# Kernel optimization log

Hardware: AMD Instinct MI355X
Metric: run time of the kernel (lower is better)

The kernel has to match this reference:

```python
import math
import jax, jax.numpy as jnp
import numpy as np

WS = 4            # window size
LS = 2 * WS       # local context size
NH = 8            # num heads
DIM = 128
EPS = 1e-5


def setup_inputs() -> dict:
    key = jax.random.key(0)
    ks = jax.random.split(key, 8)
    B, C, H, W = 4, DIM, 48, 48
    features = jax.random.normal(ks[0], (B, C, H, W), dtype=jnp.float32)
    s = 0.02
    return {
        'features': features,
        'ln_w': jnp.ones((C,), jnp.float32),
        'ln_b': jnp.zeros((C,), jnp.float32),
        'q_w': jax.random.normal(ks[1], (C, C), jnp.float32) * s,
        'q_b': jnp.zeros((C,), jnp.float32),
        'kv_w': jax.random.normal(ks[2], (2 * C, C), jnp.float32) * s,
        'kv_b': jnp.zeros((2 * C,), jnp.float32),
        'out_w': jax.random.normal(ks[3], (C, C), jnp.float32) * s,
        'out_b': jnp.zeros((C,), jnp.float32),
    }


def _avgpool_tokens(x, k):
    # x: [B,C,H,W] -> [B, (H//k)*(W//k), C]
    B, C, H, W = x.shape
    t = x.reshape(B, C, H // k, k, W // k, k).mean(axis=(3, 5))
    return t.reshape(B, C, -1).transpose(0, 2, 1)


def reference(features, ln_w, ln_b, q_w, q_b, kv_w, kv_b, out_w, out_b):
    B, C, H, W = features.shape
    Hw, Ww = H // WS, W // WS
    nw = Hw * Ww
    hd = C // NH

    # ---- window partition: [B,C,H,W] -> [B*nw, WS*WS, C]
    qt = features.reshape(B, C, Hw, WS, Ww, WS).transpose(0, 2, 4, 3, 5, 1)
    qt = qt.reshape(B * nw, WS * WS, C)

    # ---- LayerNorm(dim)
    mu = qt.mean(-1, keepdims=True)
    var = qt.var(-1, keepdims=True)
    qt = (qt - mu) / jnp.sqrt(var + EPS) * ln_w + ln_b

    # ---- local context: pad to target, unfold kernel=LS stride=WS
    target = (int(math.sqrt(nw)) - 1) * WS + LS
    ph, pw = max(0, target - H), max(0, target - W)
    pad = ((0, 0), (0, 0), (ph // 2, ph - ph // 2), (pw // 2, pw - pw // 2))
    padded = jnp.pad(features, pad)
    # channel order of patches is (C, kh, kw), same as torch unfold
    patches = jax.lax.conv_general_dilated_patches(
        padded, filter_shape=(LS, LS), window_strides=(WS, WS), padding='VALID')
    local = patches.reshape(B, C, LS * LS, nw).transpose(0, 3, 2, 1)
    local = local.reshape(B * nw, LS * LS, C)

    # ---- multi-scale pooled tokens, broadcast to each window
    mid = _avgpool_tokens(features, 2)      # [B, M, C]
    glo = _avgpool_tokens(features, 4)      # [B, G, C]
    mid = jnp.broadcast_to(mid[:, None], (B, nw) + mid.shape[1:]).reshape(B * nw, -1, C)
    glo = jnp.broadcast_to(glo[:, None], (B, nw) + glo.shape[1:]).reshape(B * nw, -1, C)

    kv_tokens = jnp.concatenate([local, mid, glo], axis=1)  # [B*nw, Nkv, C]

    # ---- projections (torch Linear: x @ W.T + b)
    queries = qt @ q_w.T + q_b
    kv = kv_tokens @ kv_w.T + kv_b
    keys, values = kv[..., :C], kv[..., C:]

    # ---- multi-head attention
    Nq, Nkv = queries.shape[1], keys.shape[1]
    q = queries.reshape(-1, Nq, NH, hd)
    k = keys.reshape(-1, Nkv, NH, hd)
    v = values.reshape(-1, Nkv, NH, hd)
    scores = jnp.einsum('bqhd,bkhd->bhqk', q, k) / math.sqrt(hd)
    weights = jax.nn.softmax(scores, axis=-1)
    attended = jnp.einsum('bhqk,bkhd->bqhd', weights, v).reshape(-1, Nq, C)

    out = attended @ out_w.T + out_b

    # ---- window reconstruction -> [B,C,H,W]
    out = out.reshape(B, Hw, Ww, WS, WS, C).transpose(0, 5, 1, 3, 2, 4)
    out = out.reshape(B, C, H, W)
    return out + features
```

## Files before the change

kernel.cpp:

```cpp
#include <hip/hip_runtime.h>


typedef unsigned short u16;
typedef short v8s __attribute__((ext_vector_type(8)));
typedef v8s __attribute__((may_alias)) v8s_am;
typedef short v4s __attribute__((ext_vector_type(4)));
typedef v4s __attribute__((may_alias)) v4s_am;
typedef float v4f __attribute__((ext_vector_type(4)));

#define MFMA_BF16(a, b, c) __builtin_amdgcn_mfma_f32_16x16x32_bf16(a, b, c, 0, 0, 0)

#if __has_builtin(__builtin_amdgcn_mfma_f32_16x16x16bf16_1k)
#define MFMA16(a, b, c) __builtin_amdgcn_mfma_f32_16x16x16bf16_1k(a, b, c, 0, 0, 0)
#else
static __device__ __forceinline__ v4f mfma16_fb(v4s a, v4s b, v4f c) {
    v8s a8 = {a[0], a[1], a[2], a[3], 0, 0, 0, 0};
    v8s b8 = {b[0], b[1], b[2], b[3], 0, 0, 0, 0};
    return MFMA_BF16(a8, b8, c);
}
#define MFMA16(a, b, c) mfma16_fb(a, b, c)
#endif

#if __has_builtin(__builtin_amdgcn_exp2f)
#define EXP2(x) __builtin_amdgcn_exp2f(x)
#else
#define EXP2(x) exp2f(x)
#endif

__device__ __forceinline__ float b2f(u16 u) {
    union { unsigned int i; float f; } x;
    x.i = ((unsigned int)u) << 16;
    return x.f;
}
__device__ __forceinline__ u16 f2b(float f) {
    union { float f; unsigned int i; } x;
    x.f = f;
    unsigned int u = x.i;
    return (u16)((u + 0x7fffu + ((u >> 16) & 1u)) >> 16);
}

__global__ __launch_bounds__(256) void k_prep(
    const float* __restrict__ F,
    const float* __restrict__ qw, const float* __restrict__ kvw,
    const float* __restrict__ ow,
    const float* __restrict__ lnw, const float* __restrict__ lnb,
    const float* __restrict__ kvb,
    u16* __restrict__ Xt, u16* __restrict__ Xln, u16* __restrict__ Wb,
    u16* __restrict__ Pml, u16* __restrict__ Vlh)
{
    int blk = blockIdx.x;
    int t = threadIdx.x;
    if (blk >= 484) {
        int base = (blk - 484) * 8192 + t * 32;
#pragma unroll
        for (int k = 0; k < 4; ++k) {
            int off = base + k * 8;
            int ch = off / 10816;
            u16 bv = f2b(kvb[128 + ch]);
            v8s o = {(short)bv, (short)bv, (short)bv, (short)bv,
                     (short)bv, (short)bv, (short)bv, (short)bv};
            *(v8s_am*)&Vlh[off] = o;
        }
        return;
    }
    if (blk >= 304) {
        int gid = (blk - 304) * 256 + t;
        int row = gid >> 4;
        int seg = gid & 15;
        v8s outv;
        if (row < 2304) {
            int b = row / 576, r = row % 576;
            int i = r / 24, j = r % 24;
#pragma unroll
            for (int jc = 0; jc < 8; ++jc) {
                int c = seg * 8 + jc;
                const float* src = F + ((size_t)(b * 128 + c)) * 2304 + (2 * i) * 48 + 2 * j;
                float2 a = *(const float2*)src;
                float2 d = *(const float2*)(src + 48);
                outv[jc] = (short)f2b((a.x + a.y + d.x + d.y) * 0.25f);
            }
        } else {
            int r2 = row - 2304;
            int b = r2 / 144, r = r2 % 144;
            int i = r / 12, j = r % 12;
#pragma unroll
            for (int jc = 0; jc < 8; ++jc) {
                int c = seg * 8 + jc;
                const float* src = F + ((size_t)(b * 128 + c)) * 2304 + (4 * i) * 48 + 4 * j;
                float s = 0.f;
#pragma unroll
                for (int di = 0; di < 4; ++di) {
                    float4 v = *(const float4*)(src + di * 48);
                    s += (v.x + v.y) + (v.z + v.w);
                }
                outv[jc] = (short)f2b(s * 0.0625f);
            }
        }
        *(v8s_am*)&Pml[((size_t)row) * 128 + seg * 8] = outv;
        return;
    }
    if (blk >= 288) {
        int base = (blk - 288) * 4096 + t * 16;
#pragma unroll
        for (int i = 0; i < 4; ++i) {
            int idx = base + i * 4;
            const float* src; int off;
            if (idx < 16384)      { src = qw;  off = idx; }
            else if (idx < 49152) { src = kvw; off = idx - 16384; }
            else                  { src = ow;  off = idx - 49152; }
            float4 v = *(const float4*)(src + off);
            unsigned long long packed =
                (unsigned long long)f2b(v.x) |
                ((unsigned long long)f2b(v.y) << 16) |
                ((unsigned long long)f2b(v.z) << 32) |
                ((unsigned long long)f2b(v.w) << 48);
            *(unsigned long long*)(Wb + idx) = packed;
        }
        if (blk == 288) {
            Wb[65536 + t] = f2b(t < 128 ? lnw[t] : lnb[t - 128]);
            Wb[65792 + t] = f2b(kvb[t]);
        }
        return;
    }
    __shared__ u16 X[128][34];
    __shared__ float Lw[128], Lb[128];
    if (t < 128) Lw[t] = lnw[t];
    else         Lb[t - 128] = lnb[t - 128];
    int b = blk / 72;
    int p0 = (blk % 72) * 32;
#pragma unroll 4
    for (int i = 0; i < 16; ++i) {
        int c = i * 8 + (t >> 5);
        int pix = t & 31;
        X[c][pix] = f2b(F[((size_t)(b * 128 + c)) * 2304 + p0 + pix]);
    }
    __syncthreads();
    int pix = t >> 3;
    int c0 = (t & 7) * 16;
    size_t row = (size_t)(b * 2304 + p0 + pix) * 128;
    float s = 0.f, s2 = 0.f;
#pragma unroll
    for (int sg = 0; sg < 2; ++sg) {
        v8s raw;
#pragma unroll
        for (int j = 0; j < 8; ++j) {
            u16 u = X[c0 + sg * 8 + j][pix];
            raw[j] = (short)u;
            float v = b2f(u);
            s += v; s2 += v * v;
        }
        *(v8s_am*)&Xt[row + c0 + sg * 8] = raw;
    }
    s += __shfl_xor(s, 1);  s2 += __shfl_xor(s2, 1);
    s += __shfl_xor(s, 2);  s2 += __shfl_xor(s2, 2);
    s += __shfl_xor(s, 4);  s2 += __shfl_xor(s2, 4);
    float mean = s * (1.f / 128.f);
    float var = s2 * (1.f / 128.f) - mean * mean;
    float rstd = rsqrtf(var + 1e-5f);
#pragma unroll
    for (int sg = 0; sg < 2; ++sg) {
        v8s o;
#pragma unroll
        for (int j = 0; j < 8; ++j) {
            int c = c0 + sg * 8 + j;
            float v = b2f(X[c][pix]);
            o[j] = (short)f2b((v - mean) * rstd * Lw[c] + Lb[c]);
        }
        *(v8s_am*)&Xln[row + c0 + sg * 8] = o;
    }
}

__global__ __launch_bounds__(256) void k_gemm_kv(
    const u16* __restrict__ Xt,
    const u16* __restrict__ Pml,
    const u16* __restrict__ W,
    const float* __restrict__ bias,
    u16* __restrict__ KVh,
    u16* __restrict__ VTg,
    u16* __restrict__ Klh,
    u16* __restrict__ Vlh)
{
    __shared__ u16 Al[64][136];
    __shared__ u16 Wl[64][136];
    int gb = blockIdx.x;
    bool loc = (gb < 144);
    int tm = loc ? gb * 64 : (gb - 144) * 64;
    int tn = blockIdx.y * 64;
    int t = threadIdx.x;
    {
        int seg = t & 15, r0 = t >> 4;
        const u16* A = loc ? Xt : Pml;
#pragma unroll
        for (int i = 0; i < 4; ++i) {
            int r = r0 + 16 * i;
            *(v8s_am*)&Al[r][seg * 8] = *(const v8s_am*)&A[((size_t)(tm + r)) * 128 + seg * 8];
            *(v8s_am*)&Wl[r][seg * 8] = *(const v8s_am*)&W[((size_t)(tn + r)) * 128 + seg * 8];
        }
    }
    __syncthreads();
    int lane = t & 63, wave = t >> 6;
    int n15 = lane & 15, quad = lane >> 4;
    int wm = (wave & 1) * 32, wn = (wave >> 1) * 32;
    v4f acc[2][2] = {};
#pragma unroll
    for (int kc = 0; kc < 4; ++kc) {
        v8s a[2], bb[2];
#pragma unroll
        for (int im = 0; im < 2; ++im)
            a[im] = *(const v8s_am*)&Al[wm + im * 16 + n15][kc * 32 + quad * 8];
#pragma unroll
        for (int in = 0; in < 2; ++in)
            bb[in] = *(const v8s_am*)&Wl[wn + in * 16 + n15][kc * 32 + quad * 8];
#pragma unroll
        for (int im = 0; im < 2; ++im)
#pragma unroll
            for (int in = 0; in < 2; ++in)
                acc[im][in] = MFMA_BF16(a[im], bb[in], acc[im][in]);
    }
    bool vdst = (tn >= 128);
    __syncthreads();
    u16* Ct = &Al[0][0];
#pragma unroll
    for (int in = 0; in < 2; ++in) {
        int nl = wn + in * 16 + n15;
        float bv = bias[tn + nl];
#pragma unroll
        for (int im = 0; im < 2; ++im) {
#pragma unroll
            for (int r = 0; r < 4; ++r) {
                int ml = wm + im * 16 + quad * 4 + r;
                u16 h = f2b(acc[im][in][r] + bv);
                Ct[vdst ? (nl * 72 + ml) : (ml * 72 + nl)] = h;
            }
        }
    }
    __syncthreads();
    {
        int a = t >> 2, sub = t & 3;
        v8s a0 = *(const v8s_am*)&Ct[a * 72 + sub * 16];
        v8s a1 = *(const v8s_am*)&Ct[a * 72 + sub * 16 + 8];
        if (!vdst) {
            int m = tm + a;
            int headc = (tn >> 4) + sub;
            size_t d; u16* dst;
            if (loc) { int b = m / 2304, px = m % 2304;
                       d = (((size_t)(headc * 4 + b)) * 2304 + px) * 16; dst = Klh; }
            else     { d = ((size_t)headc * 2880 + m) * 16; dst = KVh; }
            *(v8s_am*)&dst[d]     = a0;
            *(v8s_am*)&dst[d + 8] = a1;
        } else {
            int ch = (tn - 128) + a;
            int pxo = sub * 16;
            if (loc) {
                int b = tm / 2304;
                int s2_ = tm % 2304 + pxo;
                int hh = s2_ / 48, ww = s2_ % 48;
                size_t base = ((size_t)(ch * 4 + b)) * 2704 + (hh + 2) * 52 + ww + 2;
                union { v8s s; unsigned int u[4]; } u0, u1;
                u0.s = a0; u1.s = a1;
#pragma unroll
                for (int k = 0; k < 4; ++k) {
                    *(unsigned int*)&Vlh[base + 2 * k]     = u0.u[k];
                    *(unsigned int*)&Vlh[base + 8 + 2 * k] = u1.u[k];
                }
            } else {
                int m = tm + pxo;
                size_t base;
                if (m < 2304) { int b = m / 576, tok = m % 576;
                                base = ((size_t)(b * 128 + ch)) * 720 + tok; }
                else { int r2 = m - 2304; int b = r2 / 144, tok = 576 + r2 % 144;
                       base = ((size_t)(b * 128 + ch)) * 720 + tok; }
                *(v8s_am*)&VTg[base]     = a0;
                *(v8s_am*)&VTg[base + 8] = a1;
            }
        }
    }
}

__global__ __launch_bounds__(512, 3) void k_attn_fused(
    const float* __restrict__ F,
    const u16* __restrict__ Xln,
    const u16* __restrict__ KVh,
    const u16* __restrict__ VTg,
    const u16* __restrict__ Klh,
    const u16* __restrict__ Vlh,
    const u16* __restrict__ Wb,
    const float* __restrict__ qb,
    const float* __restrict__ ob,
    float* __restrict__ Out)
{
    __shared__ u16 KP[8][64][16];
    __shared__ u16 At[16][136];

    const u16* qwb  = Wb;
    const u16* owb  = Wb + 49152;
    const u16* kvbb = Wb + 65792;

    int blk = blockIdx.x;
    int xcd = blk & 7, jj = blk >> 3;
    int b = xcd >> 1;
    int wr = (xcd & 1) * 6 + jj / 12;
    int wc = jj % 12;

    int t = threadIdx.x;
    int lane = t & 63, wave = t >> 6, n15 = lane & 15, quad = lane >> 4;
    v4f zz4 = {0.f, 0.f, 0.f, 0.f};
    const float QSCALE = 0.25f * 1.44269504f;

    u16* KPw = &KP[wave][0][0];
    const u16* kwave = KVh + (size_t)wave * 46080;
    const u16* vrow0 = VTg + (size_t)b * 92160
                     + (size_t)(wave * 16 + n15) * 720 + quad * 4;

    int fh = lane >> 3, fw = lane & 7;
    int hh = wr * 4 - 2 + fh, ww = wc * 4 - 2 + fw;
    bool kvalid = (hh >= 0 && hh < 48 && ww >= 0 && ww < 48);
    int hc = min(max(hh, 0), 47), wcc = min(max(ww, 0), 47);
    v8s kN0, kN1;
    {
        const u16* s = Klh + ((size_t)((wave * 4 + b) * 2304 + hc * 48 + wcc)) * 16;
        kN0 = *(const v8s_am*)s; kN1 = *(const v8s_am*)(s + 8);
    }

    float fres[4];
    {
        int c = wave * 16 + n15;
#pragma unroll
        for (int r = 0; r < 4; ++r) {
            int pix = quad * 4 + r;
            int hh2 = wr * 4 + (pix >> 2), ww2 = wc * 4 + (pix & 3);
            fres[r] = F[((size_t)(b * 128 + c)) * 2304 + hh2 * 48 + ww2];
        }
    }

    int qh = wr * 4 + (n15 >> 2), qw_ = wc * 4 + (n15 & 3);
    int qpix = b * 2304 + qh * 48 + qw_;
    v8s xln[4];
#pragma unroll
    for (int kc = 0; kc < 4; ++kc)
        xln[kc] = *(const v8s_am*)&Xln[(size_t)qpix * 128 + kc * 32 + quad * 8];

    v4s qf;
    {
        int n0 = wave * 16;
        v4f qacc = zz4;
#pragma unroll
        for (int kc = 0; kc < 4; ++kc) {
            v8s aw = *(const v8s_am*)&qwb[((size_t)(n0 + n15)) * 128 + kc * 32 + quad * 8];
            qacc = MFMA_BF16(aw, xln[kc], qacc);
        }
#pragma unroll
        for (int r = 0; r < 4; ++r)
            qf[r] = (short)f2b((qacc[r] + qb[n0 + quad * 4 + r]) * QSCALE);
    }

    {
        v8s kb0 = *(const v8s_am*)&kvbb[wave * 16];
        v8s kb1 = *(const v8s_am*)&kvbb[wave * 16 + 8];
        if (!kvalid) { kN0 = kb0; kN1 = kb1; }
    }

    v4f oacc = zz4;
    float ls = 0.f;

    *(v8s_am*)&KPw[lane * 16]     = kN0;
    *(v8s_am*)&KPw[lane * 16 + 8] = kN1;
    {
        const u16* s = kwave + (size_t)(b * 576 + lane) * 16;
        kN0 = *(const v8s_am*)s; kN1 = *(const v8s_am*)(s + 8);
    }

    {
        const u16* vbaseL = Vlh + ((size_t)((wave * 16 + n15) * 4 + b)) * 2704
                          + (wr * 4 + (quad >> 1)) * 52 + wc * 4 + (quad & 1) * 4;
#pragma unroll
        for (int g = 0; g < 4; ++g) {
            v4s kf = *(const v4s_am*)&KPw[(g * 16 + n15) * 16 + quad * 4];
            v4s vf = *(const v4s_am*)(vbaseL + g * 104);
            v4f St = MFMA16(kf, qf, zz4);
            float p0 = EXP2(St[0]), p1 = EXP2(St[1]);
            float p2 = EXP2(St[2]), p3 = EXP2(St[3]);
            ls += (p0 + p1) + (p2 + p3);
            v4s pk = {(short)f2b(p0), (short)f2b(p1), (short)f2b(p2), (short)f2b(p3)};
            oacc = MFMA16(vf, pk, oacc);
        }
    }

    *(v8s_am*)&KPw[lane * 16]     = kN0;
    *(v8s_am*)&KPw[lane * 16 + 8] = kN1;
    {
        const u16* s = kwave + (size_t)(b * 576 + 64 + lane) * 16;
        kN0 = *(const v8s_am*)s; kN1 = *(const v8s_am*)(s + 8);
    }

    for (int tb = 0; tb <= 10; ++tb) {
        v4s kf[4];
#pragma unroll
        for (int g = 0; g < 4; ++g)
            kf[g] = *(const v4s_am*)&KPw[(g * 16 + n15) * 16 + quad * 4];
        *(v8s_am*)&KPw[lane * 16]     = kN0;
        *(v8s_am*)&KPw[lane * 16 + 8] = kN1;
        if (tb < 10) {
            int t2 = tb + 2;
            int row = (t2 < 9) ? (b * 576 + t2 * 64 + lane)
                               : (2304 + b * 144 + (t2 - 9) * 64 + lane);
            if (t2 == 11) row = 2304 + b * 144 + 128 + n15;
            const u16* s = kwave + (size_t)row * 16;
            kN0 = *(const v8s_am*)s; kN1 = *(const v8s_am*)(s + 8);
        }
        v4s vp[4];
#pragma unroll
        for (int g = 0; g < 4; ++g)
            vp[g] = *(const v4s_am*)(vrow0 + tb * 64 + g * 16);
#pragma unroll
        for (int g = 0; g < 4; ++g) {
            v4f St = MFMA16(kf[g], qf, zz4);
            float p0 = EXP2(St[0]), p1 = EXP2(St[1]);
            float p2 = EXP2(St[2]), p3 = EXP2(St[3]);
            ls += (p0 + p1) + (p2 + p3);
            v4s pk = {(short)f2b(p0), (short)f2b(p1), (short)f2b(p2), (short)f2b(p3)};
            oacc = MFMA16(vp[g], pk, oacc);
        }
    }
    {
        v4s kf = *(const v4s_am*)&KPw[n15 * 16 + quad * 4];
        v4s vf = *(const v4s_am*)(vrow0 + 704);
        v4f St = MFMA16(kf, qf, zz4);
        float p0 = EXP2(St[0]), p1 = EXP2(St[1]);
        float p2 = EXP2(St[2]), p3 = EXP2(St[3]);
        ls += (p0 + p1) + (p2 + p3);
        v4s pk = {(short)f2b(p0), (short)f2b(p1), (short)f2b(p2), (short)f2b(p3)};
        oacc = MFMA16(vf, pk, oacc);
    }

    ls += __shfl_xor(ls, 16);
    ls += __shfl_xor(ls, 32);
    {
        float inv = 1.f / ls;
        v4s a4 = {(short)f2b(oacc[0] * inv), (short)f2b(oacc[1] * inv),
                  (short)f2b(oacc[2] * inv), (short)f2b(oacc[3] * inv)};
        *(v4s_am*)&At[n15][wave * 16 + quad * 4] = a4;
    }
    __syncthreads();

    {
        int n0 = wave * 16;
        v4f oa = zz4;
#pragma unroll
        for (int kc = 0; kc < 4; ++kc) {
            v8s af = *(const v8s_am*)&At[n15][kc * 32 + quad * 8];
            v8s bf = *(const v8s_am*)&owb[((size_t)(n0 + n15)) * 128 + kc * 32 + quad * 8];
            oa = MFMA_BF16(af, bf, oa);
        }
        int c = n0 + n15;
        float bv = ob[c];
#pragma unroll
        for (int r = 0; r < 4; ++r) {
            int pix = quad * 4 + r;
            int hh2 = wr * 4 + (pix >> 2), ww2 = wc * 4 + (pix & 3);
            size_t idx = ((size_t)(b * 128 + c)) * 2304 + hh2 * 48 + ww2;
            Out[idx] = oa[r] + bv + fres[r];
        }
    }
}

extern "C" void kernel_launch(void* const* d_in, const int* in_sizes, int n_in,
                              void* d_out, int out_size, void* d_ws, size_t ws_size,
                              hipStream_t stream)
{
    const float* F   = (const float*)d_in[0];
    const float* lnw = (const float*)d_in[1];
    const float* lnb = (const float*)d_in[2];
    const float* qw  = (const float*)d_in[3];
    const float* qb  = (const float*)d_in[4];
    const float* kvw = (const float*)d_in[5];
    const float* kvb = (const float*)d_in[6];
    const float* ow  = (const float*)d_in[7];
    const float* ob  = (const float*)d_in[8];
    float* Out = (float*)d_out;

    u16* ws    = (u16*)d_ws;
    u16* Xt    = ws;
    u16* Xln   = Xt + 9216 * 128;
    u16* Pml   = Xln + 9216 * 128;
    u16* KVh   = Pml + 2880 * 128;
    u16* VTg   = KVh + 8 * 2880 * 16;
    u16* Klh   = VTg + 4 * 128 * 720;
    u16* Vlh   = Klh + 8 * 4 * 2304 * 16;
    u16* Wb    = Vlh + 128 * 4 * 2704;
    u16* kvwb = Wb + 16384;

    k_prep<<<653, 256, 0, stream>>>(F, qw, kvw, ow, lnw, lnb, kvb,
                                    Xt, Xln, Wb, Pml, Vlh);
    k_gemm_kv<<<dim3(189, 4), 256, 0, stream>>>(Xt, Pml, kvwb, kvb,
                                                KVh, VTg, Klh, Vlh);
    k_attn_fused<<<576, 512, 0, stream>>>(F, Xln, KVh, VTg, Klh, Vlh,
                                          Wb, qb, ob, Out);
}
```

Measured before the change: 118.6 us.

## Split attention KV loop across two wave halves per head with LDS reduction

Doubles the attention block to 1024 threads so each head is handled by two waves, each covering about half of the key/value tiles. The two partial outputs and softmax sums are combined through shared memory before normalization and the output projection. This aims to shorten the serial per-wave KV loop and raise parallelism, at the cost of duplicated Q projection work, an extra barrier, more LDS, and half the waves idling during the output projection.

```diff
diff --git a/kernel.cpp b/kernel.cpp
--- a/kernel.cpp
+++ b/kernel.cpp
@@ -277,7 +277,7 @@
     }
 }
 
-__global__ __launch_bounds__(512, 3) void k_attn_fused(
+__global__ __launch_bounds__(1024, 2) void k_attn_fused(
     const float* __restrict__ F,
     const u16* __restrict__ Xln,
     const u16* __restrict__ KVh,
@@ -289,8 +289,9 @@
     const float* __restrict__ ob,
     float* __restrict__ Out)
 {
-    __shared__ u16 KP[8][64][16];
+    __shared__ u16 KP[16][64][16];
     __shared__ u16 At[16][136];
+    __shared__ float Pb[8][64][5];
 
     const u16* qwb  = Wb;
     const u16* owb  = Wb + 49152;
@@ -304,79 +305,155 @@
 
     int t = threadIdx.x;
     int lane = t & 63, wave = t >> 6, n15 = lane & 15, quad = lane >> 4;
+    int head = wave & 7, half = wave >> 3;
     v4f zz4 = {0.f, 0.f, 0.f, 0.f};
     const float QSCALE = 0.25f * 1.44269504f;
 
     u16* KPw = &KP[wave][0][0];
-    const u16* kwave = KVh + (size_t)wave * 46080;
+    const u16* kwave = KVh + (size_t)head * 46080;
     const u16* vrow0 = VTg + (size_t)b * 92160
-                     + (size_t)(wave * 16 + n15) * 720 + quad * 4;
-
-    int fh = lane >> 3, fw = lane & 7;
-    int hh = wr * 4 - 2 + fh, ww = wc * 4 - 2 + fw;
-    bool kvalid = (hh >= 0 && hh < 48 && ww >= 0 && ww < 48);
-    int hc = min(max(hh, 0), 47), wcc = min(max(ww, 0), 47);
+                     + (size_t)(head * 16 + n15) * 720 + quad * 4;
+
     v8s kN0, kN1;
-    {
-        const u16* s = Klh + ((size_t)((wave * 4 + b) * 2304 + hc * 48 + wcc)) * 16;
+    bool kvalid = true;
+    float fres[4] = {0.f, 0.f, 0.f, 0.f};
+    if (half == 0) {
+        int fh = lane >> 3, fw = lane & 7;
+        int hh = wr * 4 - 2 + fh, ww = wc * 4 - 2 + fw;
+        kvalid = (hh >= 0 && hh < 48 && ww >= 0 && ww < 48);
+        int hc = min(max(hh, 0), 47), wcc = min(max(ww, 0), 47);
+        const u16* s = Klh + ((size_t)((head * 4 + b) * 2304 + hc * 48 + wcc)) * 16;
         kN0 = *(const v8s_am*)s; kN1 = *(const v8s_am*)(s + 8);
-    }
-
-    float fres[4];
-    {
-        int c = wave * 16 + n15;
+        int c = head * 16 + n15;
 #pragma unroll
         for (int r = 0; r < 4; ++r) {
             int pix = quad * 4 + r;
             int hh2 = wr * 4 + (pix >> 2), ww2 = wc * 4 + (pix & 3);
             fres[r] = F[((size_t)(b * 128 + c)) * 2304 + hh2 * 48 + ww2];
         }
+    } else {
+        const u16* s = kwave + (size_t)(b * 576 + 5 * 64 + lane) * 16;
+        kN0 = *(const v8s_am*)s; kN1 = *(const v8s_am*)(s + 8);
     }
 
     int qh = wr * 4 + (n15 >> 2), qw_ = wc * 4 + (n15 & 3);
     int qpix = b * 2304 + qh * 48 + qw_;
-    v8s xln[4];
-#pragma unroll
-    for (int kc = 0; kc < 4; ++kc)
-        xln[kc] = *(const v8s_am*)&Xln[(size_t)qpix * 128 + kc * 32 + quad * 8];
-
     v4s qf;
     {
-        int n0 = wave * 16;
         v4f qacc = zz4;
 #pragma unroll
         for (int kc = 0; kc < 4; ++kc) {
-            v8s aw = *(const v8s_am*)&qwb[((size_t)(n0 + n15)) * 128 + kc * 32 + quad * 8];
-            qacc = MFMA_BF16(aw, xln[kc], qacc);
+            v8s x  = *(const v8s_am*)&Xln[(size_t)qpix * 128 + kc * 32 + quad * 8];
+            v8s aw = *(const v8s_am*)&qwb[((size_t)(head * 16 + n15)) * 128 + kc * 32 + quad * 8];
+            qacc = MFMA_BF16(aw, x, qacc);
         }
 #pragma unroll
         for (int r = 0; r < 4; ++r)
-            qf[r] = (short)f2b((qacc[r] + qb[n0 + quad * 4 + r]) * QSCALE);
-    }
-
-    {
-        v8s kb0 = *(const v8s_am*)&kvbb[wave * 16];
-        v8s kb1 = *(const v8s_am*)&kvbb[wave * 16 + 8];
-        if (!kvalid) { kN0 = kb0; kN1 = kb1; }
+            qf[r] = (short)f2b((qacc[r] + qb[head * 16 + quad * 4 + r]) * QSCALE);
     }
 
     v4f oacc = zz4;
     float ls = 0.f;
 
-    *(v8s_am*)&KPw[lane * 16]     = kN0;
-    *(v8s_am*)&KPw[lane * 16 + 8] = kN1;
-    {
-        const u16* s = kwave + (size_t)(b * 576 + lane) * 16;
-        kN0 = *(const v8s_am*)s; kN1 = *(const v8s_am*)(s + 8);
-    }
-
-    {
-        const u16* vbaseL = Vlh + ((size_t)((wave * 16 + n15) * 4 + b)) * 2704
-                          + (wr * 4 + (quad >> 1)) * 52 + wc * 4 + (quad & 1) * 4;
-#pragma unroll
-        for (int g = 0; g < 4; ++g) {
-            v4s kf = *(const v4s_am*)&KPw[(g * 16 + n15) * 16 + quad * 4];
-            v4s vf = *(const v4s_am*)(vbaseL + g * 104);
+    if (half == 0) {
+        {
+            v8s kb0 = *(const v8s_am*)&kvbb[head * 16];
+            v8s kb1 = *(const v8s_am*)&kvbb[head * 16 + 8];
+            if (!kvalid) { kN0 = kb0; kN1 = kb1; }
+        }
+        *(v8s_am*)&KPw[lane * 16]     = kN0;
+        *(v8s_am*)&KPw[lane * 16 + 8] = kN1;
+        {
+            const u16* s = kwave + (size_t)(b * 576 + lane) * 16;
+            kN0 = *(const v8s_am*)s; kN1 = *(const v8s_am*)(s + 8);
+        }
+        {
+            const u16* vbaseL = Vlh + ((size_t)((head * 16 + n15) * 4 + b)) * 2704
+                              + (wr * 4 + (quad >> 1)) * 52 + wc * 4 + (quad & 1) * 4;
+#pragma unroll
+            for (int g = 0; g < 4; ++g) {
+                v4s kf = *(const v4s_am*)&KPw[(g * 16 + n15) * 16 + quad * 4];
+                v4s vf = *(const v4s_am*)(vbaseL + g * 104);
+                v4f St = MFMA16(kf, qf, zz4);
+                float p0 = EXP2(St[0]), p1 = EXP2(St[1]);
+                float p2 = EXP2(St[2]), p3 = EXP2(St[3]);
+                ls += (p0 + p1) + (p2 + p3);
+                v4s pk = {(short)f2b(p0), (short)f2b(p1), (short)f2b(p2), (short)f2b(p3)};
+                oacc = MFMA16(vf, pk, oacc);
+            }
+        }
+        *(v8s_am*)&KPw[lane * 16]     = kN0;
+        *(v8s_am*)&KPw[lane * 16 + 8] = kN1;
+        {
+            const u16* s = kwave + (size_t)(b * 576 + 64 + lane) * 16;
+            kN0 = *(const v8s_am*)s; kN1 = *(const v8s_am*)(s + 8);
+        }
+        for (int tb = 0; tb <= 4; ++tb) {
+            v4s kf[4];
+#pragma unroll
+            for (int g = 0; g < 4; ++g)
+                kf[g] = *(const v4s_am*)&KPw[(g * 16 + n15) * 16 + quad * 4];
+            if (tb < 4) {
+                *(v8s_am*)&KPw[lane * 16]     = kN0;
+                *(v8s_am*)&KPw[lane * 16 + 8] = kN1;
+                if (tb < 3) {
+                    const u16* s = kwave + (size_t)(b * 576 + (tb + 2) * 64 + lane) * 16;
+                    kN0 = *(const v8s_am*)s; kN1 = *(const v8s_am*)(s + 8);
+                }
+            }
+            v4s vp[4];
+#pragma unroll
+            for (int g = 0; g < 4; ++g)
+                vp[g] = *(const v4s_am*)(vrow0 + tb * 64 + g * 16);
+#pragma unroll
+            for (int g = 0; g < 4; ++g) {
+                v4f St = MFMA16(kf[g], qf, zz4);
+                float p0 = EXP2(St[0]), p1 = EXP2(St[1]);
+                float p2 = EXP2(St[2]), p3 = EXP2(St[3]);
+                ls += (p0 + p1) + (p2 + p3);
+                v4s pk = {(short)f2b(p0), (short)f2b(p1), (short)f2b(p2), (short)f2b(p3)};
+                oacc = MFMA16(vp[g], pk, oacc);
+            }
+        }
+    } else {
+        *(v8s_am*)&KPw[lane * 16]     = kN0;
+        *(v8s_am*)&KPw[lane * 16 + 8] = kN1;
+        {
+            const u16* s = kwave + (size_t)(b * 576 + 6 * 64 + lane) * 16;
+            kN0 = *(const v8s_am*)s; kN1 = *(const v8s_am*)(s + 8);
+        }
+        for (int tb = 5; tb <= 10; ++tb) {
+            v4s kf[4];
+#pragma unroll
+            for (int g = 0; g < 4; ++g)
+                kf[g] = *(const v4s_am*)&KPw[(g * 16 + n15) * 16 + quad * 4];
+            *(v8s_am*)&KPw[lane * 16]     = kN0;
+            *(v8s_am*)&KPw[lane * 16 + 8] = kN1;
+            if (tb <= 9) {
+                int t2 = tb + 2;
+                int row = (t2 < 9) ? (b * 576 + t2 * 64 + lane)
+                                   : (2304 + b * 144 + (t2 - 9) * 64 + lane);
+                if (t2 == 11) row = 2304 + b * 144 + 128 + n15;
+                const u16* s = kwave + (size_t)row * 16;
+                kN0 = *(const v8s_am*)s; kN1 = *(const v8s_am*)(s + 8);
+            }
+            v4s vp[4];
+#pragma unroll
+            for (int g = 0; g < 4; ++g)
+                vp[g] = *(const v4s_am*)(vrow0 + tb * 64 + g * 16);
+#pragma unroll
+            for (int g = 0; g < 4; ++g) {
+                v4f St = MFMA16(kf[g], qf, zz4);
+                float p0 = EXP2(St[0]), p1 = EXP2(St[1]);
+                float p2 = EXP2(St[2]), p3 = EXP2(St[3]);
+                ls += (p0 + p1) + (p2 + p3);
+                v4s pk = {(short)f2b(p0), (short)f2b(p1), (short)f2b(p2), (short)f2b(p3)};
+                oacc = MFMA16(vp[g], pk, oacc);
+            }
+        }
+        {
+            v4s kf = *(const v4s_am*)&KPw[n15 * 16 + quad * 4];
+            v4s vf = *(const v4s_am*)(vrow0 + 704);
             v4f St = MFMA16(kf, qf, zz4);
             float p0 = EXP2(St[0]), p1 = EXP2(St[1]);
             float p2 = EXP2(St[2]), p3 = EXP2(St[3]);
@@ -384,67 +461,26 @@
             v4s pk = {(short)f2b(p0), (short)f2b(p1), (short)f2b(p2), (short)f2b(p3)};
             oacc = MFMA16(vf, pk, oacc);
         }
-    }
-
-    *(v8s_am*)&KPw[lane * 16]     = kN0;
-    *(v8s_am*)&KPw[lane * 16 + 8] = kN1;
-    {
-        const u16* s = kwave + (size_t)(b * 576 + 64 + lane) * 16;
-        kN0 = *(const v8s_am*)s; kN1 = *(const v8s_am*)(s + 8);
-    }
-
-    for (int tb = 0; tb <= 10; ++tb) {
-        v4s kf[4];
-#pragma unroll
-        for (int g = 0; g < 4; ++g)
-            kf[g] = *(const v4s_am*)&KPw[(g * 16 + n15) * 16 + quad * 4];
-        *(v8s_am*)&KPw[lane * 16]     = kN0;
-        *(v8s_am*)&KPw[lane * 16 + 8] = kN1;
-        if (tb < 10) {
-            int t2 = tb + 2;
-            int row = (t2 < 9) ? (b * 576 + t2 * 64 + lane)
-                               : (2304 + b * 144 + (t2 - 9) * 64 + lane);
-            if (t2 == 11) row = 2304 + b * 144 + 128 + n15;
-            const u16* s = kwave + (size_t)row * 16;
-            kN0 = *(const v8s_am*)s; kN1 = *(const v8s_am*)(s + 8);
-        }
-        v4s vp[4];
-#pragma unroll
-        for (int g = 0; g < 4; ++g)
-            vp[g] = *(const v4s_am*)(vrow0 + tb * 64 + g * 16);
-#pragma unroll
-        for (int g = 0; g < 4; ++g) {
-            v4f St = MFMA16(kf[g], qf, zz4);
-            float p0 = EXP2(St[0]), p1 = EXP2(St[1]);
-            float p2 = EXP2(St[2]), p3 = EXP2(St[3]);
-            ls += (p0 + p1) + (p2 + p3);
-            v4s pk = {(short)f2b(p0), (short)f2b(p1), (short)f2b(p2), (short)f2b(p3)};
-            oacc = MFMA16(vp[g], pk, oacc);
-        }
-    }
-    {
-        v4s kf = *(const v4s_am*)&KPw[n15 * 16 + quad * 4];
-        v4s vf = *(const v4s_am*)(vrow0 + 704);
-        v4f St = MFMA16(kf, qf, zz4);
-        float p0 = EXP2(St[0]), p1 = EXP2(St[1]);
-        float p2 = EXP2(St[2]), p3 = EXP2(St[3]);
-        ls += (p0 + p1) + (p2 + p3);
-        v4s pk = {(short)f2b(p0), (short)f2b(p1), (short)f2b(p2), (short)f2b(p3)};
-        oacc = MFMA16(vf, pk, oacc);
-    }
-
-    ls += __shfl_xor(ls, 16);
-    ls += __shfl_xor(ls, 32);
-    {
+        float* p = &Pb[head][lane][0];
+        p[0] = oacc[0]; p[1] = oacc[1]; p[2] = oacc[2]; p[3] = oacc[3]; p[4] = ls;
+    }
+    __syncthreads();
+
+    if (half == 0) {
+        const float* p = &Pb[head][lane][0];
+        oacc[0] += p[0]; oacc[1] += p[1]; oacc[2] += p[2]; oacc[3] += p[3];
+        ls += p[4];
+        ls += __shfl_xor(ls, 16);
+        ls += __shfl_xor(ls, 32);
         float inv = 1.f / ls;
         v4s a4 = {(short)f2b(oacc[0] * inv), (short)f2b(oacc[1] * inv),
                   (short)f2b(oacc[2] * inv), (short)f2b(oacc[3] * inv)};
-        *(v4s_am*)&At[n15][wave * 16 + quad * 4] = a4;
+        *(v4s_am*)&At[n15][head * 16 + quad * 4] = a4;
     }
     __syncthreads();
 
-    {
-        int n0 = wave * 16;
+    if (half == 0) {
+        int n0 = head * 16;
         v4f oa = zz4;
 #pragma unroll
         for (int kc = 0; kc < 4; ++kc) {
@@ -494,6 +530,6 @@
                                     Xt, Xln, Wb, Pml, Vlh);
     k_gemm_kv<<<dim3(189, 4), 256, 0, stream>>>(Xt, Pml, kvwb, kvb,
                                                 KVh, VTg, Klh, Vlh);
-    k_attn_fused<<<576, 512, 0, stream>>>(F, Xln, KVh, VTg, Klh, Vlh,
-                                          Wb, qb, ob, Out);
-}
+    k_attn_fused<<<576, 1024, 0, stream>>>(F, Xln, KVh, VTg, Klh, Vlh,
+                                           Wb, qb, ob, Out);
+}
```

Result: slower. 126.3 us (+6.5%).
